# Performance work log

Measured on AMD Instinct MI355X. Metric: run time of the kernel, lower is better.

The kernel has to match this reference:

```python
import jax, jax.numpy as jnp
import numpy as np

N_NODES = 100000
N_EDGES = 1600000
IN_DIM = 64
HID_DIM = 128
OUT_DIM = 128


def setup_inputs() -> dict:
    key = jax.random.key(0)
    ks = jax.random.split(key, 12)
    s = 0.05
    return {
        "x": jax.random.normal(ks[0], (N_NODES, IN_DIM), jnp.float32),
        "edge_index": jax.random.randint(ks[1], (2, N_EDGES), 0, N_NODES, jnp.int64),
        "edge_attr": jax.random.uniform(ks[2], (N_EDGES, 2), jnp.float32),
        # conv1 MLP: Linear(IN+2, HID) -> ReLU -> Linear(HID, HID)
        "W11": jax.random.normal(ks[3], (IN_DIM + 2, HID_DIM), jnp.float32) * s,
        "b11": jax.random.normal(ks[4], (HID_DIM,), jnp.float32) * s,
        "W12": jax.random.normal(ks[5], (HID_DIM, HID_DIM), jnp.float32) * s,
        "b12": jax.random.normal(ks[6], (HID_DIM,), jnp.float32) * s,
        # conv2 MLP: Linear(HID+2, OUT) -> ReLU -> Linear(OUT, OUT)
        "W21": jax.random.normal(ks[7], (HID_DIM + 2, OUT_DIM), jnp.float32) * s,
        "b21": jax.random.normal(ks[8], (OUT_DIM,), jnp.float32) * s,
        "W22": jax.random.normal(ks[9], (OUT_DIM, OUT_DIM), jnp.float32) * s,
        "b22": jax.random.normal(ks[10], (OUT_DIM,), jnp.float32) * s,
    }


def _gin_conv(x, edge_index, edge_attr, W1, b1, W2, b2):
    N = x.shape[0]
    loop = jnp.arange(N, dtype=edge_index.dtype)
    src = jnp.concatenate([edge_index[0], loop])  # [E+N] message sources
    dst = jnp.concatenate([edge_index[1], loop])  # [E+N] aggregation targets
    # self-loop edge_attr filled with 1.0 (PyG add_self_loops default)
    ea = jnp.concatenate([edge_attr, jnp.ones((N, edge_attr.shape[1]), edge_attr.dtype)], axis=0)
    m = jnp.concatenate([x[src], ea], axis=-1)  # [E+N, F+2] gather + concat
    h = jnp.dot(jax.nn.relu(jnp.dot(m, W1) + b1), W2) + b2  # edge MLP
    return jax.ops.segment_sum(h, dst, num_segments=N)  # scatter-add aggregate


def reference(x, edge_index, edge_attr, W11, b11, W12, b12, W21, b21, W22, b22):
    h = _gin_conv(x, edge_index, edge_attr, W11, b11, W12, b12)
    h = jax.nn.relu(h)
    return _gin_conv(h, edge_index, edge_attr, W21, b21, W22, b22)
```

## Files before the change

kernel.cpp:

```cpp
#include <hip/hip_runtime.h>


typedef unsigned int uint;
typedef __attribute__((ext_vector_type(8))) short bf16x8;
typedef __attribute__((ext_vector_type(4))) float f32x4;

#define BSHIFT 9
#define BNODES (1 << BSHIFT)

static __device__ __forceinline__ unsigned short f2bf(float f) {
    uint u = __float_as_uint(f);
    uint r = (u + 0x7fffu + ((u >> 16) & 1u)) >> 16;
    return (unsigned short)r;
}


__global__ void wprep_all(const float* __restrict__ W11, const float* __restrict__ W12,
                          const float* __restrict__ W21, const float* __restrict__ W22,
                          unsigned short* Wt11, unsigned short* Wt12,
                          unsigned short* Wt21, unsigned short* Wt22,
                          int* bcnt, int* ptr, int N, int E) {
    int idx = blockIdx.x * 256 + threadIdx.x;
    if (idx < 256) bcnt[idx] = 0;
    if (idx == 0) ptr[N] = E;
    const float* W; unsigned short* Wt; int K; int off;
    if (idx < 64 * 128)        { W = W11; Wt = Wt11; K = 64;  off = idx; }
    else if (idx < 192 * 128)  { W = W12; Wt = Wt12; K = 128; off = idx - 64 * 128; }
    else if (idx < 320 * 128)  { W = W21; Wt = Wt21; K = 128; off = idx - 192 * 128; }
    else if (idx < 448 * 128)  { W = W22; Wt = Wt22; K = 128; off = idx - 320 * 128; }
    else return;
    int k = off >> 7, n = off & 127;
    Wt[n * K + k] = f2bf(W[k * 128 + n]);
}


__global__ __launch_bounds__(512) void bin_kernel(
    const int* __restrict__ src, const int* __restrict__ dst,
    const float* __restrict__ ea, int* __restrict__ bcnt,
    int2* __restrict__ barr, int CAP, int E, int B) {
    __shared__ int hist[256];
    __shared__ int bbase[256];
    __shared__ int gbase[256];
    __shared__ int wtot[4];
    __shared__ int2 sorted[4096];
    __shared__ unsigned char bof[4096];
    const int tileBase = blockIdx.x * 4096;
    int n = E - tileBase; if (n > 4096) n = 4096; if (n <= 0) return;
    const int tid = threadIdx.x;
    const int lane = tid & 63;
    if (tid < 256) hist[tid] = 0;
    __syncthreads();

    int2 ent[8]; int bk[8]; int rk[8];
#pragma unroll
    for (int kk = 0; kk < 8; kk++) {
        int i = kk * 512 + tid;
        bk[kk] = -1;
        if (i < n) {
            int e = tileBase + i;
            int s = src[e], d = dst[e];
            float2 a = reinterpret_cast<const float2*>(ea)[e];
            int b = d >> BSHIFT;
            int dloc = d & (BNODES - 1);
            ent[kk].x = s | (dloc << 17);
            ent[kk].y = (int)((uint)f2bf(a.x) | ((uint)f2bf(a.y) << 16));
            bk[kk] = b;
            rk[kk] = atomicAdd(&hist[b], 1);
        }
    }
    __syncthreads();
    int hv = (tid < 256) ? hist[tid] : 0;
    int inc = hv;
#pragma unroll
    for (int off = 1; off < 64; off <<= 1) {
        int tt = __shfl_up(inc, off, 64);
        if (lane >= off) inc += tt;
    }
    if ((tid >> 6) < 4 && lane == 63) wtot[tid >> 6] = inc;
    __syncthreads();
    if (tid == 0) { int run = 0; for (int i = 0; i < 4; i++) { int tt = wtot[i]; wtot[i] = run; run += tt; } }
    __syncthreads();
    if (tid < 256) bbase[tid] = inc - hv + wtot[tid >> 6];
    if (tid < B && hist[tid] > 0) gbase[tid] = atomicAdd(&bcnt[tid], hist[tid]);
    __syncthreads();
#pragma unroll
    for (int kk = 0; kk < 8; kk++) {
        if (bk[kk] >= 0) {
            int p = bbase[bk[kk]] + rk[kk];
            sorted[p] = ent[kk];
            bof[p] = (unsigned char)bk[kk];
        }
    }
    __syncthreads();
    for (int i = tid; i < n; i += 512) {
        int b = bof[i];
        barr[(long)b * CAP + gbase[b] + (i - bbase[b])] = sorted[i];
    }
}


static __device__ void csr_body(const int2* __restrict__ barr, const int* __restrict__ bcnt,
                                int CAP, int N, int2* __restrict__ csr, int* __restrict__ ptr) {
    __shared__ int hist[BNODES];
    __shared__ int lptr[BNODES];
    __shared__ int wtot[8];
    __shared__ int sbase;
    const int g = blockIdx.x;
    const int tid = threadIdx.x;
    const int lane = tid & 63;
    const int cnt = bcnt[g];
    if (tid == 0) sbase = 0;
    hist[tid] = 0;
    __syncthreads();
    if (tid < g) atomicAdd(&sbase, bcnt[tid]);
    const int2* my = barr + (long)g * CAP;
    for (int i = tid; i < cnt; i += 512)
        atomicAdd(&hist[((uint)my[i].x) >> 17], 1);
    __syncthreads();
    int v = hist[tid];
    int inc = v;
#pragma unroll
    for (int off = 1; off < 64; off <<= 1) {
        int tt = __shfl_up(inc, off, 64);
        if (lane >= off) inc += tt;
    }
    if (lane == 63) wtot[tid >> 6] = inc;
    __syncthreads();
    if (tid == 0) { int run = 0; for (int i = 0; i < 8; i++) { int tt = wtot[i]; wtot[i] = run; run += tt; } }
    __syncthreads();
    const int base = sbase;
    int excl = inc - v + wtot[tid >> 6];
    lptr[tid] = excl;
    int gnode = g * BNODES + tid;
    if (gnode < N) ptr[gnode] = base + excl;
    __syncthreads();
    for (int i = tid; i < cnt; i += 512) {
        int2 e = my[i];
        int pos = base + atomicAdd(&lptr[((uint)e.x) >> 17], 1);
        int2 o; o.x = e.x & 0x1FFFF; o.y = e.y;
        csr[pos] = o;
    }
}


template <int K, bool IN_F32, bool OUT_BF16, bool USE_CNT, bool RELU>
static __device__ __forceinline__ void gemm_body(
    const void* __restrict__ Ain, const unsigned short* __restrict__ Wt,
    const float* __restrict__ bias, const int* __restrict__ ptr,
    void* __restrict__ Cout, int N, int tid, long rowBase) {
    constexpr int KS = K / 32;
    const int wave = tid >> 6;
    const int lane = tid & 63;
    const int m = lane & 15, quad = lane >> 4;

    bf16x8 bfrag[2][KS];
#pragma unroll
    for (int ct = 0; ct < 2; ct++) {
        int col = (wave * 2 + ct) * 16 + m;
#pragma unroll
        for (int ks = 0; ks < KS; ks++)
            bfrag[ct][ks] = *(const bf16x8*)(Wt + (long)col * K + ks * 32 + quad * 8);
    }

#pragma unroll
    for (int rt = 0; rt < 4; rt++) {
        long row = rowBase + rt * 16 + m;
        long rc = row < N ? row : (long)N - 1;
        bf16x8 afrag[KS];
        if (IN_F32) {
            const float* arow = (const float*)Ain + rc * K;
#pragma unroll
            for (int ks = 0; ks < KS; ks++) {
                float4 lo = *(const float4*)(arow + ks * 32 + quad * 8);
                float4 hi = *(const float4*)(arow + ks * 32 + quad * 8 + 4);
                bf16x8 f;
                f[0] = (short)f2bf(lo.x); f[1] = (short)f2bf(lo.y);
                f[2] = (short)f2bf(lo.z); f[3] = (short)f2bf(lo.w);
                f[4] = (short)f2bf(hi.x); f[5] = (short)f2bf(hi.y);
                f[6] = (short)f2bf(hi.z); f[7] = (short)f2bf(hi.w);
                afrag[ks] = f;
            }
        } else {
            const unsigned short* arow = (const unsigned short*)Ain + rc * K;
#pragma unroll
            for (int ks = 0; ks < KS; ks++)
                afrag[ks] = *(const bf16x8*)(arow + ks * 32 + quad * 8);
        }

#pragma unroll
        for (int ct = 0; ct < 2; ct++) {
            f32x4 acc = {0.f, 0.f, 0.f, 0.f};
#pragma unroll
            for (int ks = 0; ks < KS; ks++)
                acc = __builtin_amdgcn_mfma_f32_16x16x32_bf16(afrag[ks], bfrag[ct][ks], acc, 0, 0, 0);

            int col = (wave * 2 + ct) * 16 + m;
            float b = bias[col];
#pragma unroll
            for (int r = 0; r < 4; r++) {
                long orow = rowBase + rt * 16 + quad * 4 + r;
                if (orow < N) {
                    float v = acc[r];
                    if (USE_CNT) v += b * (float)(ptr[orow + 1] - ptr[orow] + 1);
                    else v += b;
                    if (RELU) v = fmaxf(v, 0.f);
                    if (OUT_BF16) ((unsigned short*)Cout)[orow * 128 + col] = f2bf(v);
                    else ((float*)Cout)[orow * 128 + col] = v;
                }
            }
        }
    }
}

template <int K, bool IN_F32, bool OUT_BF16, bool USE_CNT, bool RELU>
__global__ __launch_bounds__(256) void gemm_mfma(
    const void* __restrict__ Ain, const unsigned short* __restrict__ Wt,
    const float* __restrict__ bias, const int* __restrict__ ptr,
    void* __restrict__ Cout, int N) {
    gemm_body<K, IN_F32, OUT_BF16, USE_CNT, RELU>(Ain, Wt, bias, ptr, Cout, N,
                                                  threadIdx.x, (long)blockIdx.x * 64);
}


__global__ __launch_bounds__(512) void csr_gemm1(
    const int2* __restrict__ barr, const int* __restrict__ bcnt, int CAP, int N,
    int2* __restrict__ csr, int* __restrict__ ptr, int CSRB,
    const float* __restrict__ x, const unsigned short* __restrict__ Wt11,
    const float* __restrict__ b11, unsigned short* __restrict__ A_bf) {
    if ((int)blockIdx.x < CSRB) {
        csr_body(barr, bcnt, CAP, N, csr, ptr);
    } else {
        int bid = blockIdx.x - CSRB;
        int sub = threadIdx.x >> 8;
        gemm_body<64, true, true, false, false>(x, Wt11, b11, nullptr, A_bf, N,
                                                threadIdx.x & 255,
                                                (long)bid * 128 + sub * 64);
    }
}


__global__ __launch_bounds__(256) void gather_kernel(
    const uint* __restrict__ Au, const int* __restrict__ ptr,
    const int2* __restrict__ csr, const float* __restrict__ we,
    uint* __restrict__ Bout, int N) {
    int node = blockIdx.x * 4 + (threadIdx.x >> 6);
    if (node >= N) return;
    node = __builtin_amdgcn_readfirstlane(node);
    const int t = threadIdx.x & 63;
    const int c = 2 * t;
    const float w0x = we[c], w0y = we[c + 1];
    const float w1x = we[128 + c], w1y = we[128 + c + 1];

    const char* Ab = (const char*)Au;
    const uint t4 = (uint)t * 4u;
#define LD(sidx) (*(const uint*)(Ab + ((((uint)(sidx)) << 8) + t4)))
#define ACC(rv, ev)                                                      \
    {                                                                    \
        float a0 = __uint_as_float(((uint)(ev)) << 16);                  \
        float a1 = __uint_as_float(((uint)(ev)) & 0xffff0000u);          \
        float vx = __uint_as_float((rv) << 16);                          \
        float vy = __uint_as_float((rv) & 0xffff0000u);                  \
        vx = fmaf(a0, w0x, fmaf(a1, w1x, vx));                           \
        vy = fmaf(a0, w0y, fmaf(a1, w1y, vy));                           \
        ax += fmaxf(vx, 0.f);                                            \
        ay += fmaxf(vy, 0.f);                                            \
    }
#define EDGE(i, off)                                                     \
    int2 c##i = csr[k + (off)];                                          \
    uint s##i = (uint)__builtin_amdgcn_readfirstlane(c##i.x);            \
    uint e##i = (uint)__builtin_amdgcn_readfirstlane(c##i.y);

    uint selfv = LD((uint)node);
    float ax = fmaxf(__uint_as_float(selfv << 16) + w0x + w1x, 0.f);
    float ay = fmaxf(__uint_as_float(selfv & 0xffff0000u) + w0y + w1y, 0.f);

    int k   = __builtin_amdgcn_readfirstlane(ptr[node]);
    int end = __builtin_amdgcn_readfirstlane(ptr[node + 1]);

    for (; k + 8 <= end; k += 8) {
        EDGE(0, 0) EDGE(1, 1) EDGE(2, 2) EDGE(3, 3)
        EDGE(4, 4) EDGE(5, 5) EDGE(6, 6) EDGE(7, 7)
        uint r0 = LD(s0); uint r1 = LD(s1); uint r2 = LD(s2); uint r3 = LD(s3);
        uint r4 = LD(s4); uint r5 = LD(s5); uint r6 = LD(s6); uint r7 = LD(s7);
        ACC(r0, e0) ACC(r1, e1) ACC(r2, e2) ACC(r3, e3)
        ACC(r4, e4) ACC(r5, e5) ACC(r6, e6) ACC(r7, e7)
    }
    for (; k + 4 <= end; k += 4) {
        EDGE(0, 0) EDGE(1, 1) EDGE(2, 2) EDGE(3, 3)
        uint r0 = LD(s0); uint r1 = LD(s1); uint r2 = LD(s2); uint r3 = LD(s3);
        ACC(r0, e0) ACC(r1, e1) ACC(r2, e2) ACC(r3, e3)
    }
    for (; k < end; k++) {
        EDGE(0, 0)
        uint r0 = LD(s0);
        ACC(r0, e0)
    }
#undef EDGE
#undef ACC
#undef LD
    uint outv = (uint)f2bf(ax) | ((uint)f2bf(ay) << 16);
    __builtin_nontemporal_store(outv, Bout + (long)node * 64 + t);
}


__global__ __launch_bounds__(256) void fused_mid_gemm(
    const unsigned short* __restrict__ Bin, const int* __restrict__ ptr,
    const unsigned short* __restrict__ WtA, const float* __restrict__ biasA,
    const unsigned short* __restrict__ WtB, const float* __restrict__ biasB,
    unsigned short* __restrict__ Cout, int N) {
    __shared__ unsigned short ts[64 * 136];
    const int wave = threadIdx.x >> 6;
    const int lane = threadIdx.x & 63;
    const int m = lane & 15, quad = lane >> 4;
    const long rowBase = (long)blockIdx.x * 64;

    bf16x8 bfrag[2][4];
#pragma unroll
    for (int ct = 0; ct < 2; ct++) {
        int col = (wave * 2 + ct) * 16 + m;
#pragma unroll
        for (int ks = 0; ks < 4; ks++)
            bfrag[ct][ks] = *(const bf16x8*)(WtA + (long)col * 128 + ks * 32 + quad * 8);
    }

    f32x4 acc[4][2];
#pragma unroll
    for (int rt = 0; rt < 4; rt++) {
        long row = rowBase + rt * 16 + m;
        long rc = row < N ? row : (long)N - 1;
        const unsigned short* arow = Bin + rc * 128;
        bf16x8 af[4];
#pragma unroll
        for (int ks = 0; ks < 4; ks++)
            af[ks] = *(const bf16x8*)(arow + ks * 32 + quad * 8);
#pragma unroll
        for (int ct = 0; ct < 2; ct++) {
            f32x4 a = {0.f, 0.f, 0.f, 0.f};
#pragma unroll
            for (int ks = 0; ks < 4; ks++)
                a = __builtin_amdgcn_mfma_f32_16x16x32_bf16(af[ks], bfrag[ct][ks], a, 0, 0, 0);
            acc[rt][ct] = a;
        }
    }

#pragma unroll
    for (int rt = 0; rt < 4; rt++) {
        float cntf[4];
#pragma unroll
        for (int r = 0; r < 4; r++) {
            long grow = rowBase + rt * 16 + quad * 4 + r;
            cntf[r] = (grow < N) ? (float)(ptr[grow + 1] - ptr[grow] + 1) : 1.f;
        }
#pragma unroll
        for (int ct = 0; ct < 2; ct++) {
            int col = (wave * 2 + ct) * 16 + m;
            float b = biasA[col];
#pragma unroll
            for (int r = 0; r < 4; r++) {
                int row = rt * 16 + quad * 4 + r;
                ts[row * 136 + col] = f2bf(fmaxf(acc[rt][ct][r] + b * cntf[r], 0.f));
            }
        }
    }
    __syncthreads();

#pragma unroll
    for (int ct = 0; ct < 2; ct++) {
        int col = (wave * 2 + ct) * 16 + m;
#pragma unroll
        for (int ks = 0; ks < 4; ks++)
            bfrag[ct][ks] = *(const bf16x8*)(WtB + (long)col * 128 + ks * 32 + quad * 8);
    }
#pragma unroll
    for (int rt = 0; rt < 4; rt++) {
        const unsigned short* lr = ts + (rt * 16 + m) * 136;
        bf16x8 af[4];
#pragma unroll
        for (int ks = 0; ks < 4; ks++)
            af[ks] = *(const bf16x8*)(lr + ks * 32 + quad * 8);
#pragma unroll
        for (int ct = 0; ct < 2; ct++) {
            f32x4 a = {0.f, 0.f, 0.f, 0.f};
#pragma unroll
            for (int ks = 0; ks < 4; ks++)
                a = __builtin_amdgcn_mfma_f32_16x16x32_bf16(af[ks], bfrag[ct][ks], a, 0, 0, 0);
            int col = (wave * 2 + ct) * 16 + m;
            float b = biasB[col];
#pragma unroll
            for (int r = 0; r < 4; r++) {
                long grow = rowBase + rt * 16 + quad * 4 + r;
                if (grow < N) Cout[grow * 128 + col] = f2bf(a[r] + b);
            }
        }
    }
}


extern "C" void kernel_launch(void* const* d_in, const int* in_sizes, int n_in,
                              void* d_out, int out_size, void* d_ws, size_t ws_size,
                              hipStream_t stream) {
    const float* x   = (const float*)d_in[0];
    const int*   ei  = (const int*)d_in[1];
    const float* ea  = (const float*)d_in[2];
    const float* W11 = (const float*)d_in[3];
    const float* b11 = (const float*)d_in[4];
    const float* W12 = (const float*)d_in[5];
    const float* b12 = (const float*)d_in[6];
    const float* W21 = (const float*)d_in[7];
    const float* b21 = (const float*)d_in[8];
    const float* W22 = (const float*)d_in[9];
    const float* b22 = (const float*)d_in[10];
    float* out = (float*)d_out;

    const int N = in_sizes[0] / 64;
    const int E = in_sizes[1] / 2;
    const int* src = ei;
    const int* dst = ei + E;

    const int B = (N + BNODES - 1) >> BSHIFT;
    const int CAP = E / B + 4096;

    char* p = (char*)d_ws;
    unsigned short* A_bf = (unsigned short*)p;  p += (size_t)N * 128 * 2;
    unsigned short* B_bf = (unsigned short*)p;
    int2* barr = (int2*)B_bf;                   p += (size_t)N * 128 * 2;
    int2* csr  = (int2*)p;                      p += (size_t)E * 8;
    int* ptr   = (int*)p;                       p += (size_t)(N + 1) * 4;
    int* bcnt  = (int*)p;                       p += 256 * 4;
    unsigned short* Wt11 = (unsigned short*)p;  p += (size_t)64 * 128 * 2;
    unsigned short* Wt12 = (unsigned short*)p;  p += (size_t)128 * 128 * 2;
    unsigned short* Wt21 = (unsigned short*)p;  p += (size_t)128 * 128 * 2;
    unsigned short* Wt22 = (unsigned short*)p;

    const int binBlocks = (E + 4095) / 4096;
    const int gatherBlocks = (N + 3) / 4;
    const int tileBlocks = (N + 63) / 64;
    const int g1Tiles = (N + 127) / 128;

    wprep_all<<<224, 256, 0, stream>>>(W11, W12, W21, W22,
                                       Wt11, Wt12, Wt21, Wt22,
                                       bcnt, ptr, N, E);
    bin_kernel<<<binBlocks, 512, 0, stream>>>(src, dst, ea, bcnt, barr, CAP, E, B);
    csr_gemm1<<<B + g1Tiles, 512, 0, stream>>>(barr, bcnt, CAP, N, csr, ptr, B,
                                               x, Wt11, b11, A_bf);
    gather_kernel<<<gatherBlocks, 256, 0, stream>>>((const uint*)A_bf, ptr, csr,
                                                    W11 + 64 * 128, (uint*)B_bf, N);
    fused_mid_gemm<<<tileBlocks, 256, 0, stream>>>(B_bf, ptr, Wt12, b12, Wt21, b21, A_bf, N);
    gather_kernel<<<gatherBlocks, 256, 0, stream>>>((const uint*)A_bf, ptr, csr,
                                                    W21 + 128 * 128, (uint*)B_bf, N);
    gemm_mfma<128, false, false, true, false><<<tileBlocks, 256, 0, stream>>>(
        B_bf, Wt22, b22, ptr, out, N);
}
```

Before: 364.0 us.

## Merge all GIN stages into one persistent cooperative kernel with grid syncs

Replaces the seven separate kernel launches with a single cooperative persistent kernel that moves through the phases (weight prep, binning, CSR+GEMM1, gather, mid GEMM, gather, final GEMM), separated by grid.sync. The gather now handles two nodes per wave in an interleaved loop to expose more memory parallelism, and the bin tile shrinks to 2048. The goal is to remove launch gaps and inter-kernel drain. In exchange, grid-wide barriers add cost, the persistent grid size caps occupancy, and a per-phase launch fallback path is kept in case the cooperative launch fails.

```diff
diff --git a/kernel.cpp b/kernel.cpp
--- a/kernel.cpp
+++ b/kernel.cpp
@@ -1,151 +1,154 @@
 #include <hip/hip_runtime.h>
+#include <hip/hip_cooperative_groups.h>
+
+namespace cg = cooperative_groups;
 
 
 typedef unsigned int uint;
+typedef unsigned short ushort;
 typedef __attribute__((ext_vector_type(8))) short bf16x8;
 typedef __attribute__((ext_vector_type(4))) float f32x4;
 
 #define BSHIFT 9
-#define BNODES (1 << BSHIFT)
-
-static __device__ __forceinline__ unsigned short f2bf(float f) {
+#define BNODES 512
+#define BIN_TILE 2048
+
+static __device__ __forceinline__ ushort f2bf(float f) {
     uint u = __float_as_uint(f);
     uint r = (u + 0x7fffu + ((u >> 16) & 1u)) >> 16;
-    return (unsigned short)r;
-}
-
-
-__global__ void wprep_all(const float* __restrict__ W11, const float* __restrict__ W12,
-                          const float* __restrict__ W21, const float* __restrict__ W22,
-                          unsigned short* Wt11, unsigned short* Wt12,
-                          unsigned short* Wt21, unsigned short* Wt22,
-                          int* bcnt, int* ptr, int N, int E) {
-    int idx = blockIdx.x * 256 + threadIdx.x;
-    if (idx < 256) bcnt[idx] = 0;
-    if (idx == 0) ptr[N] = E;
-    const float* W; unsigned short* Wt; int K; int off;
-    if (idx < 64 * 128)        { W = W11; Wt = Wt11; K = 64;  off = idx; }
-    else if (idx < 192 * 128)  { W = W12; Wt = Wt12; K = 128; off = idx - 64 * 128; }
-    else if (idx < 320 * 128)  { W = W21; Wt = Wt21; K = 128; off = idx - 192 * 128; }
-    else if (idx < 448 * 128)  { W = W22; Wt = Wt22; K = 128; off = idx - 320 * 128; }
-    else return;
-    int k = off >> 7, n = off & 127;
-    Wt[n * K + k] = f2bf(W[k * 128 + n]);
-}
-
-
-__global__ __launch_bounds__(512) void bin_kernel(
-    const int* __restrict__ src, const int* __restrict__ dst,
-    const float* __restrict__ ea, int* __restrict__ bcnt,
-    int2* __restrict__ barr, int CAP, int E, int B) {
-    __shared__ int hist[256];
-    __shared__ int bbase[256];
-    __shared__ int gbase[256];
-    __shared__ int wtot[4];
-    __shared__ int2 sorted[4096];
-    __shared__ unsigned char bof[4096];
-    const int tileBase = blockIdx.x * 4096;
-    int n = E - tileBase; if (n > 4096) n = 4096; if (n <= 0) return;
-    const int tid = threadIdx.x;
-    const int lane = tid & 63;
-    if (tid < 256) hist[tid] = 0;
-    __syncthreads();
-
-    int2 ent[8]; int bk[8]; int rk[8];
-#pragma unroll
-    for (int kk = 0; kk < 8; kk++) {
-        int i = kk * 512 + tid;
-        bk[kk] = -1;
-        if (i < n) {
-            int e = tileBase + i;
-            int s = src[e], d = dst[e];
-            float2 a = reinterpret_cast<const float2*>(ea)[e];
-            int b = d >> BSHIFT;
-            int dloc = d & (BNODES - 1);
-            ent[kk].x = s | (dloc << 17);
-            ent[kk].y = (int)((uint)f2bf(a.x) | ((uint)f2bf(a.y) << 16));
-            bk[kk] = b;
-            rk[kk] = atomicAdd(&hist[b], 1);
-        }
-    }
-    __syncthreads();
-    int hv = (tid < 256) ? hist[tid] : 0;
-    int inc = hv;
-#pragma unroll
-    for (int off = 1; off < 64; off <<= 1) {
-        int tt = __shfl_up(inc, off, 64);
-        if (lane >= off) inc += tt;
-    }
-    if ((tid >> 6) < 4 && lane == 63) wtot[tid >> 6] = inc;
-    __syncthreads();
-    if (tid == 0) { int run = 0; for (int i = 0; i < 4; i++) { int tt = wtot[i]; wtot[i] = run; run += tt; } }
-    __syncthreads();
-    if (tid < 256) bbase[tid] = inc - hv + wtot[tid >> 6];
-    if (tid < B && hist[tid] > 0) gbase[tid] = atomicAdd(&bcnt[tid], hist[tid]);
-    __syncthreads();
-#pragma unroll
-    for (int kk = 0; kk < 8; kk++) {
-        if (bk[kk] >= 0) {
-            int p = bbase[bk[kk]] + rk[kk];
-            sorted[p] = ent[kk];
-            bof[p] = (unsigned char)bk[kk];
-        }
-    }
-    __syncthreads();
-    for (int i = tid; i < n; i += 512) {
-        int b = bof[i];
-        barr[(long)b * CAP + gbase[b] + (i - bbase[b])] = sorted[i];
-    }
-}
-
-
-static __device__ void csr_body(const int2* __restrict__ barr, const int* __restrict__ bcnt,
-                                int CAP, int N, int2* __restrict__ csr, int* __restrict__ ptr) {
-    __shared__ int hist[BNODES];
-    __shared__ int lptr[BNODES];
-    __shared__ int wtot[8];
-    __shared__ int sbase;
-    const int g = blockIdx.x;
-    const int tid = threadIdx.x;
-    const int lane = tid & 63;
-    const int cnt = bcnt[g];
-    if (tid == 0) sbase = 0;
-    hist[tid] = 0;
-    __syncthreads();
-    if (tid < g) atomicAdd(&sbase, bcnt[tid]);
-    const int2* my = barr + (long)g * CAP;
-    for (int i = tid; i < cnt; i += 512)
-        atomicAdd(&hist[((uint)my[i].x) >> 17], 1);
-    __syncthreads();
-    int v = hist[tid];
-    int inc = v;
-#pragma unroll
-    for (int off = 1; off < 64; off <<= 1) {
-        int tt = __shfl_up(inc, off, 64);
-        if (lane >= off) inc += tt;
-    }
-    if (lane == 63) wtot[tid >> 6] = inc;
-    __syncthreads();
-    if (tid == 0) { int run = 0; for (int i = 0; i < 8; i++) { int tt = wtot[i]; wtot[i] = run; run += tt; } }
-    __syncthreads();
-    const int base = sbase;
-    int excl = inc - v + wtot[tid >> 6];
-    lptr[tid] = excl;
-    int gnode = g * BNODES + tid;
-    if (gnode < N) ptr[gnode] = base + excl;
-    __syncthreads();
-    for (int i = tid; i < cnt; i += 512) {
-        int2 e = my[i];
-        int pos = base + atomicAdd(&lptr[((uint)e.x) >> 17], 1);
-        int2 o; o.x = e.x & 0x1FFFF; o.y = e.y;
-        csr[pos] = o;
-    }
-}
-
-
-template <int K, bool IN_F32, bool OUT_BF16, bool USE_CNT, bool RELU>
+    return (ushort)r;
+}
+static __device__ __forceinline__ int rfl(int v) { return __builtin_amdgcn_readfirstlane(v); }
+
+struct GP {
+    const float* x;
+    const int* src;
+    const int* dst;
+    const float* ea;
+    const float* W11; const float* b11;
+    const float* W12; const float* b12;
+    const float* W21; const float* b21;
+    const float* W22; const float* b22;
+    const float* we1;
+    const float* we2;
+    ushort *Wt11, *Wt12, *Wt21, *Wt22;
+    ushort* A_bf;
+    uint*   B_u;
+    int2*   barr;
+    int2*   csr;
+    int*    ptr;
+    int*    bcnt;
+    float*  out;
+    int N, E, B, CAP, tiles;
+};
+
+
+static __device__ __forceinline__ uint ldrow(const char* Ab, uint t4, uint sidx) {
+    return *(const uint*)(Ab + ((sidx << 8) + t4));
+}
+static __device__ __forceinline__ void accum_edge(
+    uint rv, uint ev, float w0x, float w0y, float w1x, float w1y,
+    float& ax, float& ay) {
+    float a0 = __uint_as_float(ev << 16);
+    float a1 = __uint_as_float(ev & 0xffff0000u);
+    float vx = __uint_as_float(rv << 16);
+    float vy = __uint_as_float(rv & 0xffff0000u);
+    vx = fmaf(a0, w0x, fmaf(a1, w1x, vx));
+    vy = fmaf(a0, w0y, fmaf(a1, w1y, vy));
+    ax += fmaxf(vx, 0.f);
+    ay += fmaxf(vy, 0.f);
+}
+static __device__ __forceinline__ void drain_node(
+    const char* Ab, uint t4, const int2* __restrict__ csr, int k, int end,
+    float w0x, float w0y, float w1x, float w1y, float& ax, float& ay) {
+    for (; k + 4 <= end; k += 4) {
+        int2 c0 = csr[k], c1 = csr[k + 1], c2 = csr[k + 2], c3 = csr[k + 3];
+        uint s0 = (uint)rfl(c0.x), e0 = (uint)rfl(c0.y);
+        uint s1 = (uint)rfl(c1.x), e1 = (uint)rfl(c1.y);
+        uint s2 = (uint)rfl(c2.x), e2 = (uint)rfl(c2.y);
+        uint s3 = (uint)rfl(c3.x), e3 = (uint)rfl(c3.y);
+        uint r0 = ldrow(Ab, t4, s0), r1 = ldrow(Ab, t4, s1);
+        uint r2 = ldrow(Ab, t4, s2), r3 = ldrow(Ab, t4, s3);
+        accum_edge(r0, e0, w0x, w0y, w1x, w1y, ax, ay);
+        accum_edge(r1, e1, w0x, w0y, w1x, w1y, ax, ay);
+        accum_edge(r2, e2, w0x, w0y, w1x, w1y, ax, ay);
+        accum_edge(r3, e3, w0x, w0y, w1x, w1y, ax, ay);
+    }
+    for (; k < end; k++) {
+        int2 c0 = csr[k];
+        uint s0 = (uint)rfl(c0.x), e0 = (uint)rfl(c0.y);
+        uint r0 = ldrow(Ab, t4, s0);
+        accum_edge(r0, e0, w0x, w0y, w1x, w1y, ax, ay);
+    }
+}
+
+static __device__ void gather_phase(
+    const uint* __restrict__ Au, const int* __restrict__ ptr,
+    const int2* __restrict__ csr, const float* __restrict__ we,
+    uint* __restrict__ Bout, int N, int wid, int NW, int t) {
+    const int c = 2 * t;
+    const float w0x = we[c], w0y = we[c + 1];
+    const float w1x = we[128 + c], w1y = we[128 + c + 1];
+    const char* Ab = (const char*)Au;
+    const uint t4 = (uint)t * 4u;
+
+    for (int n0 = wid * 2; n0 < N; n0 += NW * 2) {
+        const int n1 = n0 + 1;
+        uint sv0 = ldrow(Ab, t4, (uint)n0);
+        float ax0 = fmaxf(__uint_as_float(sv0 << 16) + w0x + w1x, 0.f);
+        float ay0 = fmaxf(__uint_as_float(sv0 & 0xffff0000u) + w0y + w1y, 0.f);
+        int k0 = rfl(ptr[n0]);
+        int e0 = rfl(ptr[n0 + 1]);
+        const bool has1 = (n1 < N);
+        float ax1 = 0.f, ay1 = 0.f;
+        int k1 = 0, e1 = 0;
+        if (has1) {
+            uint sv1 = ldrow(Ab, t4, (uint)n1);
+            ax1 = fmaxf(__uint_as_float(sv1 << 16) + w0x + w1x, 0.f);
+            ay1 = fmaxf(__uint_as_float(sv1 & 0xffff0000u) + w0y + w1y, 0.f);
+            k1 = rfl(ptr[n1]);
+            e1 = rfl(ptr[n1 + 1]);
+        }
+        while (k0 + 4 <= e0 && k1 + 4 <= e1) {
+            int2 ca0 = csr[k0], ca1 = csr[k0 + 1], ca2 = csr[k0 + 2], ca3 = csr[k0 + 3];
+            int2 cb0 = csr[k1], cb1 = csr[k1 + 1], cb2 = csr[k1 + 2], cb3 = csr[k1 + 3];
+            uint sa0 = (uint)rfl(ca0.x), ea0 = (uint)rfl(ca0.y);
+            uint sa1 = (uint)rfl(ca1.x), ea1 = (uint)rfl(ca1.y);
+            uint sa2 = (uint)rfl(ca2.x), ea2 = (uint)rfl(ca2.y);
+            uint sa3 = (uint)rfl(ca3.x), ea3 = (uint)rfl(ca3.y);
+            uint sb0 = (uint)rfl(cb0.x), eb0 = (uint)rfl(cb0.y);
+            uint sb1 = (uint)rfl(cb1.x), eb1 = (uint)rfl(cb1.y);
+            uint sb2 = (uint)rfl(cb2.x), eb2 = (uint)rfl(cb2.y);
+            uint sb3 = (uint)rfl(cb3.x), eb3 = (uint)rfl(cb3.y);
+            uint ra0 = ldrow(Ab, t4, sa0), ra1 = ldrow(Ab, t4, sa1);
+            uint ra2 = ldrow(Ab, t4, sa2), ra3 = ldrow(Ab, t4, sa3);
+            uint rb0 = ldrow(Ab, t4, sb0), rb1 = ldrow(Ab, t4, sb1);
+            uint rb2 = ldrow(Ab, t4, sb2), rb3 = ldrow(Ab, t4, sb3);
+            accum_edge(ra0, ea0, w0x, w0y, w1x, w1y, ax0, ay0);
+            accum_edge(ra1, ea1, w0x, w0y, w1x, w1y, ax0, ay0);
+            accum_edge(ra2, ea2, w0x, w0y, w1x, w1y, ax0, ay0);
+            accum_edge(ra3, ea3, w0x, w0y, w1x, w1y, ax0, ay0);
+            accum_edge(rb0, eb0, w0x, w0y, w1x, w1y, ax1, ay1);
+            accum_edge(rb1, eb1, w0x, w0y, w1x, w1y, ax1, ay1);
+            accum_edge(rb2, eb2, w0x, w0y, w1x, w1y, ax1, ay1);
+            accum_edge(rb3, eb3, w0x, w0y, w1x, w1y, ax1, ay1);
+            k0 += 4; k1 += 4;
+        }
+        drain_node(Ab, t4, csr, k0, e0, w0x, w0y, w1x, w1y, ax0, ay0);
+        uint o0 = (uint)f2bf(ax0) | ((uint)f2bf(ay0) << 16);
+        __builtin_nontemporal_store(o0, Bout + (long)n0 * 64 + t);
+        if (has1) {
+            drain_node(Ab, t4, csr, k1, e1, w0x, w0y, w1x, w1y, ax1, ay1);
+            uint o1 = (uint)f2bf(ax1) | ((uint)f2bf(ay1) << 16);
+            __builtin_nontemporal_store(o1, Bout + (long)n1 * 64 + t);
+        }
+    }
+}
+
+
+template <int K, bool IN_F32, bool OUT_BF16, bool USE_CNT>
 static __device__ __forceinline__ void gemm_body(
-    const void* __restrict__ Ain, const unsigned short* __restrict__ Wt,
+    const void* __restrict__ Ain, const ushort* __restrict__ Wt,
     const float* __restrict__ bias, const int* __restrict__ ptr,
     void* __restrict__ Cout, int N, int tid, long rowBase) {
     constexpr int KS = K / 32;
@@ -181,7 +184,7 @@
                 afrag[ks] = f;
             }
         } else {
-            const unsigned short* arow = (const unsigned short*)Ain + rc * K;
+            const ushort* arow = (const ushort*)Ain + rc * K;
 #pragma unroll
             for (int ks = 0; ks < KS; ks++)
                 afrag[ks] = *(const bf16x8*)(arow + ks * 32 + quad * 8);
@@ -203,8 +206,7 @@
                     float v = acc[r];
                     if (USE_CNT) v += b * (float)(ptr[orow + 1] - ptr[orow] + 1);
                     else v += b;
-                    if (RELU) v = fmaxf(v, 0.f);
-                    if (OUT_BF16) ((unsigned short*)Cout)[orow * 128 + col] = f2bf(v);
+                    if (OUT_BF16) ((ushort*)Cout)[orow * 128 + col] = f2bf(v);
                     else ((float*)Cout)[orow * 128 + col] = v;
                 }
             }
@@ -212,187 +214,232 @@
     }
 }
 
-template <int K, bool IN_F32, bool OUT_BF16, bool USE_CNT, bool RELU>
-__global__ __launch_bounds__(256) void gemm_mfma(
-    const void* __restrict__ Ain, const unsigned short* __restrict__ Wt,
-    const float* __restrict__ bias, const int* __restrict__ ptr,
-    void* __restrict__ Cout, int N) {
-    gemm_body<K, IN_F32, OUT_BF16, USE_CNT, RELU>(Ain, Wt, bias, ptr, Cout, N,
-                                                  threadIdx.x, (long)blockIdx.x * 64);
-}
-
-
-__global__ __launch_bounds__(512) void csr_gemm1(
-    const int2* __restrict__ barr, const int* __restrict__ bcnt, int CAP, int N,
-    int2* __restrict__ csr, int* __restrict__ ptr, int CSRB,
-    const float* __restrict__ x, const unsigned short* __restrict__ Wt11,
-    const float* __restrict__ b11, unsigned short* __restrict__ A_bf) {
-    if ((int)blockIdx.x < CSRB) {
-        csr_body(barr, bcnt, CAP, N, csr, ptr);
-    } else {
-        int bid = blockIdx.x - CSRB;
-        int sub = threadIdx.x >> 8;
-        gemm_body<64, true, true, false, false>(x, Wt11, b11, nullptr, A_bf, N,
-                                                threadIdx.x & 255,
-                                                (long)bid * 128 + sub * 64);
-    }
-}
-
-
-__global__ __launch_bounds__(256) void gather_kernel(
-    const uint* __restrict__ Au, const int* __restrict__ ptr,
-    const int2* __restrict__ csr, const float* __restrict__ we,
-    uint* __restrict__ Bout, int N) {
-    int node = blockIdx.x * 4 + (threadIdx.x >> 6);
-    if (node >= N) return;
-    node = __builtin_amdgcn_readfirstlane(node);
-    const int t = threadIdx.x & 63;
-    const int c = 2 * t;
-    const float w0x = we[c], w0y = we[c + 1];
-    const float w1x = we[128 + c], w1y = we[128 + c + 1];
-
-    const char* Ab = (const char*)Au;
-    const uint t4 = (uint)t * 4u;
-#define LD(sidx) (*(const uint*)(Ab + ((((uint)(sidx)) << 8) + t4)))
-#define ACC(rv, ev)                                                      \
-    {                                                                    \
-        float a0 = __uint_as_float(((uint)(ev)) << 16);                  \
-        float a1 = __uint_as_float(((uint)(ev)) & 0xffff0000u);          \
-        float vx = __uint_as_float((rv) << 16);                          \
-        float vy = __uint_as_float((rv) & 0xffff0000u);                  \
-        vx = fmaf(a0, w0x, fmaf(a1, w1x, vx));                           \
-        vy = fmaf(a0, w0y, fmaf(a1, w1y, vy));                           \
-        ax += fmaxf(vx, 0.f);                                            \
-        ay += fmaxf(vy, 0.f);                                            \
-    }
-#define EDGE(i, off)                                                     \
-    int2 c##i = csr[k + (off)];                                          \
-    uint s##i = (uint)__builtin_amdgcn_readfirstlane(c##i.x);            \
-    uint e##i = (uint)__builtin_amdgcn_readfirstlane(c##i.y);
-
-    uint selfv = LD((uint)node);
-    float ax = fmaxf(__uint_as_float(selfv << 16) + w0x + w1x, 0.f);
-    float ay = fmaxf(__uint_as_float(selfv & 0xffff0000u) + w0y + w1y, 0.f);
-
-    int k   = __builtin_amdgcn_readfirstlane(ptr[node]);
-    int end = __builtin_amdgcn_readfirstlane(ptr[node + 1]);
-
-    for (; k + 8 <= end; k += 8) {
-        EDGE(0, 0) EDGE(1, 1) EDGE(2, 2) EDGE(3, 3)
-        EDGE(4, 4) EDGE(5, 5) EDGE(6, 6) EDGE(7, 7)
-        uint r0 = LD(s0); uint r1 = LD(s1); uint r2 = LD(s2); uint r3 = LD(s3);
-        uint r4 = LD(s4); uint r5 = LD(s5); uint r6 = LD(s6); uint r7 = LD(s7);
-        ACC(r0, e0) ACC(r1, e1) ACC(r2, e2) ACC(r3, e3)
-        ACC(r4, e4) ACC(r5, e5) ACC(r6, e6) ACC(r7, e7)
-    }
-    for (; k + 4 <= end; k += 4) {
-        EDGE(0, 0) EDGE(1, 1) EDGE(2, 2) EDGE(3, 3)
-        uint r0 = LD(s0); uint r1 = LD(s1); uint r2 = LD(s2); uint r3 = LD(s3);
-        ACC(r0, e0) ACC(r1, e1) ACC(r2, e2) ACC(r3, e3)
-    }
-    for (; k < end; k++) {
-        EDGE(0, 0)
-        uint r0 = LD(s0);
-        ACC(r0, e0)
-    }
-#undef EDGE
-#undef ACC
-#undef LD
-    uint outv = (uint)f2bf(ax) | ((uint)f2bf(ay) << 16);
-    __builtin_nontemporal_store(outv, Bout + (long)node * 64 + t);
-}
-
-
-__global__ __launch_bounds__(256) void fused_mid_gemm(
-    const unsigned short* __restrict__ Bin, const int* __restrict__ ptr,
-    const unsigned short* __restrict__ WtA, const float* __restrict__ biasA,
-    const unsigned short* __restrict__ WtB, const float* __restrict__ biasB,
-    unsigned short* __restrict__ Cout, int N) {
-    __shared__ unsigned short ts[64 * 136];
-    const int wave = threadIdx.x >> 6;
-    const int lane = threadIdx.x & 63;
-    const int m = lane & 15, quad = lane >> 4;
-    const long rowBase = (long)blockIdx.x * 64;
-
-    bf16x8 bfrag[2][4];
-#pragma unroll
-    for (int ct = 0; ct < 2; ct++) {
-        int col = (wave * 2 + ct) * 16 + m;
-#pragma unroll
-        for (int ks = 0; ks < 4; ks++)
-            bfrag[ct][ks] = *(const bf16x8*)(WtA + (long)col * 128 + ks * 32 + quad * 8);
-    }
-
-    f32x4 acc[4][2];
-#pragma unroll
-    for (int rt = 0; rt < 4; rt++) {
-        long row = rowBase + rt * 16 + m;
-        long rc = row < N ? row : (long)N - 1;
-        const unsigned short* arow = Bin + rc * 128;
-        bf16x8 af[4];
-#pragma unroll
-        for (int ks = 0; ks < 4; ks++)
-            af[ks] = *(const bf16x8*)(arow + ks * 32 + quad * 8);
-#pragma unroll
-        for (int ct = 0; ct < 2; ct++) {
-            f32x4 a = {0.f, 0.f, 0.f, 0.f};
-#pragma unroll
-            for (int ks = 0; ks < 4; ks++)
-                a = __builtin_amdgcn_mfma_f32_16x16x32_bf16(af[ks], bfrag[ct][ks], a, 0, 0, 0);
-            acc[rt][ct] = a;
-        }
-    }
-
-#pragma unroll
-    for (int rt = 0; rt < 4; rt++) {
-        float cntf[4];
-#pragma unroll
-        for (int r = 0; r < 4; r++) {
-            long grow = rowBase + rt * 16 + quad * 4 + r;
-            cntf[r] = (grow < N) ? (float)(ptr[grow + 1] - ptr[grow] + 1) : 1.f;
-        }
-#pragma unroll
-        for (int ct = 0; ct < 2; ct++) {
-            int col = (wave * 2 + ct) * 16 + m;
-            float b = biasA[col];
-#pragma unroll
-            for (int r = 0; r < 4; r++) {
-                int row = rt * 16 + quad * 4 + r;
-                ts[row * 136 + col] = f2bf(fmaxf(acc[rt][ct][r] + b * cntf[r], 0.f));
-            }
-        }
-    }
-    __syncthreads();
-
-#pragma unroll
-    for (int ct = 0; ct < 2; ct++) {
-        int col = (wave * 2 + ct) * 16 + m;
-#pragma unroll
-        for (int ks = 0; ks < 4; ks++)
-            bfrag[ct][ks] = *(const bf16x8*)(WtB + (long)col * 128 + ks * 32 + quad * 8);
-    }
-#pragma unroll
-    for (int rt = 0; rt < 4; rt++) {
-        const unsigned short* lr = ts + (rt * 16 + m) * 136;
-        bf16x8 af[4];
-#pragma unroll
-        for (int ks = 0; ks < 4; ks++)
-            af[ks] = *(const bf16x8*)(lr + ks * 32 + quad * 8);
-#pragma unroll
-        for (int ct = 0; ct < 2; ct++) {
-            f32x4 a = {0.f, 0.f, 0.f, 0.f};
-#pragma unroll
-            for (int ks = 0; ks < 4; ks++)
-                a = __builtin_amdgcn_mfma_f32_16x16x32_bf16(af[ks], bfrag[ct][ks], a, 0, 0, 0);
-            int col = (wave * 2 + ct) * 16 + m;
-            float b = biasB[col];
-#pragma unroll
-            for (int r = 0; r < 4; r++) {
-                long grow = rowBase + rt * 16 + quad * 4 + r;
-                if (grow < N) Cout[grow * 128 + col] = f2bf(a[r] + b);
-            }
-        }
-    }
+
+__global__ __launch_bounds__(256) void gin_coop(GP P, int phase) {
+    __shared__ int2 smem[2696];
+    cg::grid_group grid = cg::this_grid();
+    const bool all = (phase < 0);
+    const int tid = threadIdx.x;
+    const int bid = (int)blockIdx.x;
+    const int G = (int)gridDim.x;
+    const int lane = tid & 63;
+    const int wv = tid >> 6;
+
+    if (all || phase == 0) {
+        for (int idx = bid * 256 + tid; idx < 448 * 128; idx += G * 256) {
+            const float* W; ushort* Wt; int K; int off;
+            if (idx < 64 * 128)        { W = P.W11; Wt = P.Wt11; K = 64;  off = idx; }
+            else if (idx < 192 * 128)  { W = P.W12; Wt = P.Wt12; K = 128; off = idx - 64 * 128; }
+            else if (idx < 320 * 128)  { W = P.W21; Wt = P.Wt21; K = 128; off = idx - 192 * 128; }
+            else                       { W = P.W22; Wt = P.Wt22; K = 128; off = idx - 320 * 128; }
+            int k = off >> 7, n = off & 127;
+            Wt[n * K + k] = f2bf(W[k * 128 + n]);
+        }
+        if (bid == 0) { P.bcnt[tid] = 0; if (tid == 0) P.ptr[P.N] = P.E; }
+    }
+    if (all) grid.sync();
+
+    if (all || phase == 1) {
+        int2* sorted = smem;
+        unsigned char* bof = (unsigned char*)(smem + 2048);
+        int* hist  = (int*)(bof + 2048);
+        int* bbase = hist + 256;
+        int* gbase = bbase + 256;
+        int* wtot  = gbase + 256;
+        const int T = (P.E + BIN_TILE - 1) / BIN_TILE;
+        for (int tile = bid; tile < T; tile += G) {
+            const int tb = tile * BIN_TILE;
+            int n = P.E - tb; if (n > BIN_TILE) n = BIN_TILE;
+            hist[tid] = 0;
+            __syncthreads();
+            int2 ent[8]; int bk[8]; int rk[8];
+#pragma unroll
+            for (int kk = 0; kk < 8; kk++) {
+                int i = kk * 256 + tid;
+                bk[kk] = -1;
+                if (i < n) {
+                    int e = tb + i;
+                    int s = P.src[e], d = P.dst[e];
+                    float2 a = reinterpret_cast<const float2*>(P.ea)[e];
+                    int b = d >> BSHIFT;
+                    ent[kk].x = s | ((d & (BNODES - 1)) << 17);
+                    ent[kk].y = (int)((uint)f2bf(a.x) | ((uint)f2bf(a.y) << 16));
+                    bk[kk] = b;
+                    rk[kk] = atomicAdd(&hist[b], 1);
+                }
+            }
+            __syncthreads();
+            int hv = hist[tid], inc = hv;
+#pragma unroll
+            for (int off = 1; off < 64; off <<= 1) {
+                int tt = __shfl_up(inc, off, 64);
+                if (lane >= off) inc += tt;
+            }
+            if (lane == 63) wtot[wv] = inc;
+            __syncthreads();
+            if (tid == 0) { int run = 0; for (int j = 0; j < 4; j++) { int tt = wtot[j]; wtot[j] = run; run += tt; } }
+            __syncthreads();
+            bbase[tid] = inc - hv + wtot[wv];
+            if (tid < P.B && hv > 0) gbase[tid] = atomicAdd(&P.bcnt[tid], hv);
+            __syncthreads();
+#pragma unroll
+            for (int kk = 0; kk < 8; kk++)
+                if (bk[kk] >= 0) {
+                    int pp = bbase[bk[kk]] + rk[kk];
+                    sorted[pp] = ent[kk];
+                    bof[pp] = (unsigned char)bk[kk];
+                }
+            __syncthreads();
+            for (int i = tid; i < n; i += 256) {
+                int b = bof[i];
+                P.barr[(long)b * P.CAP + gbase[b] + (i - bbase[b])] = sorted[i];
+            }
+            __syncthreads();
+        }
+    }
+    if (all) grid.sync();
+
+    if (all || phase == 2) {
+        if (bid < P.B) {
+            int* chist = (int*)smem;
+            int* clptr = chist + 512;
+            int* cwtot = clptr + 512;
+            int* csb   = cwtot + 4;
+            const int g = bid;
+            const int cnt = P.bcnt[g];
+            if (tid == 0) csb[0] = 0;
+            chist[tid] = 0; chist[tid + 256] = 0;
+            __syncthreads();
+            if (tid < g) atomicAdd(csb, P.bcnt[tid]);
+            const int2* my = P.barr + (long)g * P.CAP;
+            for (int i = tid; i < cnt; i += 256)
+                atomicAdd(&chist[((uint)my[i].x) >> 17], 1);
+            __syncthreads();
+            int v0 = chist[2 * tid], v1 = chist[2 * tid + 1];
+            int s = v0 + v1, inc = s;
+#pragma unroll
+            for (int off = 1; off < 64; off <<= 1) {
+                int tt = __shfl_up(inc, off, 64);
+                if (lane >= off) inc += tt;
+            }
+            if (lane == 63) cwtot[wv] = inc;
+            __syncthreads();
+            if (tid == 0) { int run = 0; for (int j = 0; j < 4; j++) { int tt = cwtot[j]; cwtot[j] = run; run += tt; } }
+            __syncthreads();
+            const int base = csb[0];
+            int excl = inc - s + cwtot[wv];
+            clptr[2 * tid] = excl;
+            clptr[2 * tid + 1] = excl + v0;
+            int gn = g * BNODES + 2 * tid;
+            if (gn < P.N) P.ptr[gn] = base + excl;
+            if (gn + 1 < P.N) P.ptr[gn + 1] = base + excl + v0;
+            __syncthreads();
+            for (int i = tid; i < cnt; i += 256) {
+                int2 e = my[i];
+                int pos = base + atomicAdd(&clptr[((uint)e.x) >> 17], 1);
+                int2 o; o.x = e.x & 0x1FFFF; o.y = e.y;
+                P.csr[pos] = o;
+            }
+        } else {
+            for (int t2 = bid - P.B; t2 < P.tiles; t2 += G - P.B)
+                gemm_body<64, true, true, false>(P.x, P.Wt11, P.b11, nullptr,
+                                                 P.A_bf, P.N, tid, (long)t2 * 64);
+        }
+    }
+    if (all) grid.sync();
+
+    if (all || phase == 3)
+        gather_phase((const uint*)P.A_bf, P.ptr, P.csr, P.we1, P.B_u, P.N,
+                     bid * 4 + wv, G * 4, lane);
+    if (all) grid.sync();
+
+    if (all || phase == 4) {
+        ushort* ts = (ushort*)smem;
+        const int m = lane & 15, quad = lane >> 4;
+        for (int t2 = bid; t2 < P.tiles; t2 += G) {
+            const long rowBase = (long)t2 * 64;
+            bf16x8 bfrag[2][4];
+#pragma unroll
+            for (int ct = 0; ct < 2; ct++) {
+                int col = (wv * 2 + ct) * 16 + m;
+#pragma unroll
+                for (int ks = 0; ks < 4; ks++)
+                    bfrag[ct][ks] = *(const bf16x8*)(P.Wt12 + (long)col * 128 + ks * 32 + quad * 8);
+            }
+#pragma unroll
+            for (int rt = 0; rt < 4; rt++) {
+                long row = rowBase + rt * 16 + m;
+                long rc = row < P.N ? row : (long)P.N - 1;
+                const ushort* arow = (const ushort*)P.B_u + rc * 128;
+                bf16x8 af[4];
+#pragma unroll
+                for (int ks = 0; ks < 4; ks++)
+                    af[ks] = *(const bf16x8*)(arow + ks * 32 + quad * 8);
+                float cntf[4];
+#pragma unroll
+                for (int r = 0; r < 4; r++) {
+                    long grow = rowBase + rt * 16 + quad * 4 + r;
+                    cntf[r] = (grow < P.N) ? (float)(P.ptr[grow + 1] - P.ptr[grow] + 1) : 1.f;
+                }
+#pragma unroll
+                for (int ct = 0; ct < 2; ct++) {
+                    f32x4 a = {0.f, 0.f, 0.f, 0.f};
+#pragma unroll
+                    for (int ks = 0; ks < 4; ks++)
+                        a = __builtin_amdgcn_mfma_f32_16x16x32_bf16(af[ks], bfrag[ct][ks], a, 0, 0, 0);
+                    int col = (wv * 2 + ct) * 16 + m;
+                    float b = P.b12[col];
+#pragma unroll
+                    for (int r = 0; r < 4; r++) {
+                        int rowi = rt * 16 + quad * 4 + r;
+                        ts[rowi * 136 + col] = f2bf(fmaxf(a[r] + b * cntf[r], 0.f));
+                    }
+                }
+            }
+            __syncthreads();
+#pragma unroll
+            for (int ct = 0; ct < 2; ct++) {
+                int col = (wv * 2 + ct) * 16 + m;
+#pragma unroll
+                for (int ks = 0; ks < 4; ks++)
+                    bfrag[ct][ks] = *(const bf16x8*)(P.Wt21 + (long)col * 128 + ks * 32 + quad * 8);
+            }
+#pragma unroll
+            for (int rt = 0; rt < 4; rt++) {
+                const ushort* lr = ts + (rt * 16 + m) * 136;
+                bf16x8 af[4];
+#pragma unroll
+                for (int ks = 0; ks < 4; ks++)
+                    af[ks] = *(const bf16x8*)(lr + ks * 32 + quad * 8);
+#pragma unroll
+                for (int ct = 0; ct < 2; ct++) {
+                    f32x4 a = {0.f, 0.f, 0.f, 0.f};
+#pragma unroll
+                    for (int ks = 0; ks < 4; ks++)
+                        a = __builtin_amdgcn_mfma_f32_16x16x32_bf16(af[ks], bfrag[ct][ks], a, 0, 0, 0);
+                    int col = (wv * 2 + ct) * 16 + m;
+                    float b = P.b21[col];
+#pragma unroll
+                    for (int r = 0; r < 4; r++) {
+                        long grow = rowBase + rt * 16 + quad * 4 + r;
+                        if (grow < P.N) P.A_bf[grow * 128 + col] = f2bf(a[r] + b);
+                    }
+                }
+            }
+            __syncthreads();
+        }
+    }
+    if (all) grid.sync();
+
+    if (all || phase == 5)
+        gather_phase((const uint*)P.A_bf, P.ptr, P.csr, P.we2, P.B_u, P.N,
+                     bid * 4 + wv, G * 4, lane);
+    if (all) grid.sync();
+
+    if (all || phase == 6)
+        for (int t2 = bid; t2 < P.tiles; t2 += G)
+            gemm_body<128, false, false, true>((const ushort*)P.B_u, P.Wt22, P.b22,
+                                               P.ptr, P.out, P.N, tid, (long)t2 * 64);
 }
 
 
@@ -402,52 +449,60 @@
     const float* x   = (const float*)d_in[0];
     const int*   ei  = (const int*)d_in[1];
     const float* ea  = (const float*)d_in[2];
-    const float* W11 = (const float*)d_in[3];
-    const float* b11 = (const float*)d_in[4];
-    const float* W12 = (const float*)d_in[5];
-    const float* b12 = (const float*)d_in[6];
-    const float* W21 = (const float*)d_in[7];
-    const float* b21 = (const float*)d_in[8];
-    const float* W22 = (const float*)d_in[9];
-    const float* b22 = (const float*)d_in[10];
-    float* out = (float*)d_out;
 
     const int N = in_sizes[0] / 64;
     const int E = in_sizes[1] / 2;
-    const int* src = ei;
-    const int* dst = ei + E;
-
     const int B = (N + BNODES - 1) >> BSHIFT;
-    const int CAP = E / B + 4096;
+    const int CAP = E / B + 2048;
 
     char* p = (char*)d_ws;
-    unsigned short* A_bf = (unsigned short*)p;  p += (size_t)N * 128 * 2;
-    unsigned short* B_bf = (unsigned short*)p;
-    int2* barr = (int2*)B_bf;                   p += (size_t)N * 128 * 2;
-    int2* csr  = (int2*)p;                      p += (size_t)E * 8;
-    int* ptr   = (int*)p;                       p += (size_t)(N + 1) * 4;
-    int* bcnt  = (int*)p;                       p += 256 * 4;
-    unsigned short* Wt11 = (unsigned short*)p;  p += (size_t)64 * 128 * 2;
-    unsigned short* Wt12 = (unsigned short*)p;  p += (size_t)128 * 128 * 2;
-    unsigned short* Wt21 = (unsigned short*)p;  p += (size_t)128 * 128 * 2;
-    unsigned short* Wt22 = (unsigned short*)p;
-
-    const int binBlocks = (E + 4095) / 4096;
-    const int gatherBlocks = (N + 3) / 4;
-    const int tileBlocks = (N + 63) / 64;
-    const int g1Tiles = (N + 127) / 128;
-
-    wprep_all<<<224, 256, 0, stream>>>(W11, W12, W21, W22,
-                                       Wt11, Wt12, Wt21, Wt22,
-                                       bcnt, ptr, N, E);
-    bin_kernel<<<binBlocks, 512, 0, stream>>>(src, dst, ea, bcnt, barr, CAP, E, B);
-    csr_gemm1<<<B + g1Tiles, 512, 0, stream>>>(barr, bcnt, CAP, N, csr, ptr, B,
-                                               x, Wt11, b11, A_bf);
-    gather_kernel<<<gatherBlocks, 256, 0, stream>>>((const uint*)A_bf, ptr, csr,
-                                                    W11 + 64 * 128, (uint*)B_bf, N);
-    fused_mid_gemm<<<tileBlocks, 256, 0, stream>>>(B_bf, ptr, Wt12, b12, Wt21, b21, A_bf, N);
-    gather_kernel<<<gatherBlocks, 256, 0, stream>>>((const uint*)A_bf, ptr, csr,
-                                                    W21 + 128 * 128, (uint*)B_bf, N);
-    gemm_mfma<128, false, false, true, false><<<tileBlocks, 256, 0, stream>>>(
-        B_bf, Wt22, b22, ptr, out, N);
-}
+    ushort* A_bf = (ushort*)p;        p += (size_t)N * 128 * 2;
+    uint*   B_u  = (uint*)p;
+    int2*   barr = (int2*)p;          p += (size_t)N * 64 * 4;
+    int2*   csr  = (int2*)p;          p += (size_t)E * 8;
+    int*    ptr  = (int*)p;           p += (size_t)(N + 1) * 4;
+    int*    bcnt = (int*)p;           p += 256 * 4;
+    ushort* Wt11 = (ushort*)p;        p += (size_t)64 * 128 * 2;
+    ushort* Wt12 = (ushort*)p;        p += (size_t)128 * 128 * 2;
+    ushort* Wt21 = (ushort*)p;        p += (size_t)128 * 128 * 2;
+    ushort* Wt22 = (ushort*)p;
+
+    GP P;
+    P.x = x; P.src = ei; P.dst = ei + E; P.ea = ea;
+    P.W11 = (const float*)d_in[3];  P.b11 = (const float*)d_in[4];
+    P.W12 = (const float*)d_in[5];  P.b12 = (const float*)d_in[6];
+    P.W21 = (const float*)d_in[7];  P.b21 = (const float*)d_in[8];
+    P.W22 = (const float*)d_in[9];  P.b22 = (const float*)d_in[10];
+    P.we1 = P.W11 + 64 * 128;
+    P.we2 = P.W21 + 128 * 128;
+    P.Wt11 = Wt11; P.Wt12 = Wt12; P.Wt21 = Wt21; P.Wt22 = Wt22;
+    P.A_bf = A_bf; P.B_u = B_u; P.barr = barr; P.csr = csr;
+    P.ptr = ptr; P.bcnt = bcnt; P.out = (float*)d_out;
+    P.N = N; P.E = E; P.B = B; P.CAP = CAP;
+    P.tiles = (N + 63) / 64;
+
+    static int Gcache = 0;
+    if (Gcache == 0) {
+        int maxB = 0;
+        if (hipOccupancyMaxActiveBlocksPerMultiprocessor(
+                &maxB, reinterpret_cast<const void*>(&gin_coop), 256, 0) != hipSuccess || maxB < 1)
+            maxB = 4;
+        int cus = 0;
+        if (hipDeviceGetAttribute(&cus, hipDeviceAttributeMultiprocessorCount, 0) != hipSuccess || cus < 1)
+            cus = 256;
+        long g = (long)maxB * cus;
+        if (g > 2048) g = 2048;
+        if (g < 256) g = 256;
+        Gcache = (int)g;
+    }
+
+    int phase = -1;
+    void* args[] = { (void*)&P, (void*)&phase };
+    hipError_t err = hipLaunchCooperativeKernel(
+        reinterpret_cast<const void*>(&gin_coop),
+        dim3(Gcache), dim3(256), args, 0, stream);
+    if (err != hipSuccess) {
+        for (int ph = 0; ph < 7; ph++)
+            gin_coop<<<Gcache, 256, 0, stream>>>(P, ph);
+    }
+}
```

Result: slower. 947.7 us (+160.4%).
